# Kernel optimization log

Measured on AMD Instinct MI355X. Metric: run time of the kernel, lower is better.

The kernel has to match this reference:

```python
import jax, jax.numpy as jnp
import numpy as np

B = 32768   # batch (agents)
H = 64      # h_dim
E = 16      # embedding_dim
M = 6       # num_modes (n_samples)
P = M * 2   # traj_points
T = 30      # pred_len (seq_len)


def setup_inputs() -> dict:
    key = jax.random.key(0)
    ks = jax.random.split(key, 14)
    def s(k, shape, scale=0.1):
        return jax.random.normal(k, shape, jnp.float32) * scale
    return dict(
        traj_abs=s(ks[0], (1, B, 2), 1.0),
        traj_rel=s(ks[1], (1, B, 2), 1.0),
        h0=s(ks[2], (1, B, H)),
        c0=s(ks[3], (1, B, H)),
        W_ih=s(ks[4], (4 * H, E)),
        W_hh=s(ks[5], (4 * H, H)),
        b_ih=s(ks[6], (4 * H,)),
        b_hh=s(ks[7], (4 * H,)),
        W_se=s(ks[8], (E, P)),
        b_se=s(ks[9], (E,)),
        W_pos=s(ks[10], (P, H)),
        b_pos=s(ks[11], (P,)),
        W_conf=s(ks[12], (M, H)),
        b_conf=s(ks[13], (M,)),
    )


def reference(traj_abs, traj_rel, h0, c0, W_ih, W_hh, b_ih, b_hh,
              W_se, b_se, W_pos, b_pos, W_conf, b_conf):
    b = traj_rel.shape[1]
    # repeat_interleave the (x,y) pair num_modes times along feature dim -> [b, 12]
    rel12 = jnp.tile(traj_rel.reshape(b, 1, 2), (1, M, 1)).reshape(b, P)
    x = jax.nn.leaky_relu(rel12 @ W_se.T + b_se)  # [b, E]
    h = h0[0]
    c = c0[0]

    def step(carry, _):
        x, h, c = carry
        # PyTorch LSTM cell, gate order i, f, g, o
        gates = x @ W_ih.T + b_ih + h @ W_hh.T + b_hh  # [b, 4H]
        i, f, g, o = jnp.split(gates, 4, axis=-1)
        c = jax.nn.sigmoid(f) * c + jax.nn.sigmoid(i) * jnp.tanh(g)
        h = jax.nn.sigmoid(o) * jnp.tanh(c)
        rel = h @ W_pos.T + b_pos                      # [b, P]
        x = jax.nn.leaky_relu(rel @ W_se.T + b_se)     # [b, E]
        return (x, h, c), rel

    (x, h, c), rels = jax.lax.scan(step, (x, h, c), None, length=T)  # rels: [T, b, P]
    pred = rels.reshape(T, b, M, 2).transpose(1, 2, 0, 3)            # [b, M, T, 2]
    conf = jax.nn.softmax(h @ W_conf.T + b_conf, axis=1)             # [b, M]
    return pred, conf
```

## Files before the change

### kernel.cpp

```cpp
#include <hip/hip_runtime.h>
#include <hip/hip_bf16.h>

typedef _Float16 half8 __attribute__((ext_vector_type(8)));
typedef _Float16 half4 __attribute__((ext_vector_type(4)));
typedef float float4v __attribute__((ext_vector_type(4)));

#define BATCH 32768
#define TT 30

#if __has_builtin(__builtin_amdgcn_exp2f)
#define FEXP2(x) __builtin_amdgcn_exp2f(x)
#else
#define FEXP2(x) __expf((x) * 0.6931471805599453f)
#endif
#if __has_builtin(__builtin_amdgcn_rcpf)
#define FRCP(x) __builtin_amdgcn_rcpf(x)
#else
#define FRCP(x) (1.0f / (x))
#endif

#define NLOG2E  -1.4426950408889634f
#define N2LOG2E -2.8853900817779268f

#define WFRAG_OFF 0
#define WCF_OFF   12288
#define BIASB_OFF 13312
#define SXY_OFF   13568
#define CBIAS_OFF 13616
#define WCONF_OFF 13648
#define BCONF_OFF 14032
#define FLAG_IDX  14038
#define CONF_BASE (BATCH * 360)

__global__ void detect_kernel(const unsigned short* __restrict__ raw,
                              int* __restrict__ flag_out) {
    __shared__ int sflag[256];
    int local = 0;
    for (int i = threadIdx.x; i < 16384; i += 256) {
        unsigned short u = raw[i];
        if ((u & 0x7F80u) == 0x7F80u) local = 1;
    }
    sflag[threadIdx.x] = local;
    __syncthreads();
    if (threadIdx.x == 0) {
        int f = 0;
        for (int i = 0; i < 256; ++i) f |= sflag[i];
        flag_out[0] = f;
    }
}

__device__ __forceinline__ float ldin(const void* p, int i, int isf32) {
    return isf32 ? ((const float*)p)[i]
                 : (float)((const __hip_bfloat16*)p)[i];
}

__global__ void prep_kernel(const void* __restrict__ W_ih,
                            const void* __restrict__ W_hh,
                            const void* __restrict__ b_ih,
                            const void* __restrict__ b_hh,
                            const void* __restrict__ W_se,
                            const void* __restrict__ b_se,
                            const void* __restrict__ W_pos,
                            const void* __restrict__ b_pos,
                            const void* __restrict__ W_conf,
                            const void* __restrict__ b_conf,
                            float* __restrict__ ws)
{
    const int isf32 = ((const int*)(ws + FLAG_IDX))[0];
    int tid = blockIdx.x * blockDim.x + threadIdx.x;
    int stride = gridDim.x * blockDim.x;
    _Float16* wfh = (_Float16*)ws;

    for (int idx = tid; idx < 24576; idx += stride) {
        int jj = idx & 7, r = idx >> 3;
        int lane = r & 63; r >>= 6;
        int ks = r % 3; r /= 3;
        int gate = r & 3; int wv = r >> 2;
        int col = lane & 15, akq = lane >> 4;
        int k = ks * 32 + akq * 8 + jj;
        int row = gate * 64 + wv * 16 + col;
        float v = 0.f;
        if (k < 16) v = ldin(W_ih, row * 16 + k, isf32);
        else if (k < 80) v = ldin(W_hh, row * 64 + (k - 16), isf32);
        v *= (gate == 2) ? N2LOG2E : NLOG2E;
        wfh[idx] = (_Float16)v;
    }
    _Float16* wch = (_Float16*)(ws + WCF_OFF);
    for (int idx = tid; idx < 2048; idx += stride) {
        int jj = idx & 7, r = idx >> 3;
        int lane = r & 63; r >>= 6;
        int ks = r & 1, role = r >> 1;
        int col = lane & 15, akq = lane >> 4;
        int k = ks * 32 + akq * 8 + jj;
        float v = 0.f;
        if (role == 0) {
            if (col < 12) v = ldin(W_pos, col * 64 + k, isf32);
        } else {
            float s = 0.f;
            for (int p = 0; p < 12; ++p)
                s += ldin(W_se, col * 12 + p, isf32) * ldin(W_pos, p * 64 + k, isf32);
            v = s;
        }
        wch[idx] = (_Float16)v;
    }
    for (int idx = tid; idx < 256; idx += stride) {
        int gate = idx >> 6;
        float scale = (gate == 2) ? N2LOG2E : NLOG2E;
        ws[BIASB_OFF + idx] = (ldin(b_ih, idx, isf32) + ldin(b_hh, idx, isf32)) * scale;
    }
    for (int idx = tid; idx < 16; idx += stride) {
        float sx = 0.f, sy = 0.f;
        for (int m = 0; m < 6; ++m) {
            sx += ldin(W_se, idx * 12 + 2 * m, isf32);
            sy += ldin(W_se, idx * 12 + 2 * m + 1, isf32);
        }
        ws[SXY_OFF + idx * 3 + 0] = sx;
        ws[SXY_OFF + idx * 3 + 1] = sy;
        ws[SXY_OFF + idx * 3 + 2] = ldin(b_se, idx, isf32);
    }
    for (int idx = tid; idx < 32; idx += stride) {
        int w = idx >> 4, cc = idx & 15;
        float v = 0.f;
        if (w == 0) {
            if (cc < 12) v = ldin(b_pos, cc, isf32);
        } else {
            float s = ldin(b_se, cc, isf32);
            for (int p = 0; p < 12; ++p)
                s += ldin(W_se, cc * 12 + p, isf32) * ldin(b_pos, p, isf32);
            v = s;
        }
        ws[CBIAS_OFF + idx] = v;
    }
    for (int idx = tid; idx < 384; idx += stride)
        ws[WCONF_OFF + idx] = ldin(W_conf, idx, isf32);
    for (int idx = tid; idx < 6; idx += stride)
        ws[BCONF_OFF + idx] = ldin(b_conf, idx, isf32);
}

__global__ __launch_bounds__(256, 4) void lstm_kernel(
    const void* __restrict__ traj_rel,
    const void* __restrict__ h0,
    const void* __restrict__ c0,
    const float* __restrict__ ws,
    float* __restrict__ out)
{
    __shared__ _Float16 zsh[2 * 16 * 168];
    __shared__ _Float16 predh[12 * 30 * 36];

    const int tid = threadIdx.x;
    const int lane = tid & 63;
    const int wid = __builtin_amdgcn_readfirstlane(tid >> 6);
    const int role = wid & 1;
    const int col16 = lane & 15;
    const int akq = lane >> 4;
    const int base = blockIdx.x * 32;
    const int isf32 = ((const int*)(ws + FLAG_IDX))[0];

    const float4v* wfg = (const float4v*)ws;
    half8 Bf[4][3];
#pragma unroll
    for (int tl = 0; tl < 4; ++tl)
#pragma unroll
        for (int ks = 0; ks < 3; ++ks)
            Bf[tl][ks] = __builtin_bit_cast(half8,
                wfg[((wid * 4 + tl) * 3 + ks) * 64 + lane]);
    float bias4[4];
#pragma unroll
    for (int tl = 0; tl < 4; ++tl)
        bias4[tl] = ws[BIASB_OFF + tl * 64 + wid * 16 + col16];
    half8 wfc[2];
    {
        const float4v* wcg = (const float4v*)(ws + WCF_OFF);
#pragma unroll
        for (int ks = 0; ks < 2; ++ks)
            wfc[ks] = __builtin_bit_cast(half8, wcg[(role * 2 + ks) * 64 + lane]);
    }
    const float cb = ws[CBIAS_OFF + role * 16 + col16];

    int aoff[2][3];
#pragma unroll
    for (int p = 0; p < 2; ++p)
#pragma unroll
        for (int ks = 0; ks < 3; ++ks) {
            int q = ks * 4 + akq;
            int off = (q < 2) ? q * 8
                    : (q < 10) ? 32 + p * 64 + (q - 2) * 8
                               : 16 + (q - 10) * 8;
            aoff[p][ks] = col16 * 168 + off;
        }
    const int zcb = col16 * 168 + 32 + akq * 8;
    const int rb = akq * 672;
    const int hb = 32 + wid * 16 + col16;

    float cg0[4], cg1[4];
    {
        int unit = wid * 16 + col16;
#pragma unroll
        for (int i = 0; i < 4; ++i) {
            cg0[i] = ldin(c0, (base + akq * 4 + i) * 64 + unit, isf32);
            cg1[i] = ldin(c0, (base + 16 + akq * 4 + i) * 64 + unit, isf32);
        }
    }
    {
        int m = tid & 31, jq2 = tid >> 5;
        int g = m >> 4, row = m & 15;
        _Float16* zg = &zsh[g * 2688 + row * 168];
        half8 ha;
#pragma unroll
        for (int i = 0; i < 8; ++i)
            ha[i] = (_Float16)ldin(h0, (base + m) * 64 + jq2 * 8 + i, isf32);
        *(half8*)&zg[32 + jq2 * 8] = ha;
        if (jq2 < 4) {
            float rx = ldin(traj_rel, 2 * (base + m), isf32);
            float ry = ldin(traj_rel, 2 * (base + m) + 1, isf32);
            half4 xs;
#pragma unroll
            for (int i = 0; i < 4; ++i) {
                int e = 4 * jq2 + i;
                float x = fmaf(rx, ws[SXY_OFF + e * 3],
                          fmaf(ry, ws[SXY_OFF + e * 3 + 1], ws[SXY_OFF + e * 3 + 2]));
                xs[i] = (_Float16)(x > 0.f ? x : 0.01f * x);
            }
            *(half4*)&zg[4 * jq2] = xs;
        } else if (jq2 < 6) {
            half8 zz = {};
            *(half8*)&zg[16 + (jq2 - 4) * 8] = zz;
        }
    }
    __syncthreads();

    _Float16* const zg0p = &zsh[0];
    _Float16* const zg1p = &zsh[2688];

#define PHASE_AB(ZG, PC, PN, CARR) do {                                       \
    float4v acc_[4];                                                          \
    _Pragma("unroll")                                                         \
    for (int tl = 0; tl < 4; ++tl) {                                          \
        float bv = bias4[tl];                                                 \
        acc_[tl][0] = bv; acc_[tl][1] = bv; acc_[tl][2] = bv; acc_[tl][3] = bv;\
    }                                                                         \
    _Pragma("unroll")                                                         \
    for (int ks = 0; ks < 3; ++ks) {                                          \
        half8 af_ = *(const half8*)&(ZG)[aoff[PC][ks]];                       \
        _Pragma("unroll")                                                     \
        for (int tl = 0; tl < 4; ++tl)                                        \
            acc_[tl] = __builtin_amdgcn_mfma_f32_16x16x32_f16(                \
                af_, Bf[tl][ks], acc_[tl], 0, 0, 0);                          \
    }                                                                         \
    _Pragma("unroll")                                                         \
    for (int i = 0; i < 4; ++i) {                                             \
        float ei = FEXP2(acc_[0][i]);                                         \
        float ef = FEXP2(acc_[1][i]);                                         \
        float eg = FEXP2(acc_[2][i]);                                         \
        float eo = FEXP2(acc_[3][i]);                                         \
        float pp = (1.f + ei) * (1.f + eg);                                   \
        float qq = 1.f + ef;                                                  \
        float cn = fmaf((CARR)[i], pp, (1.f - eg) * qq) * FRCP(pp * qq);      \
        (CARR)[i] = cn;                                                       \
        float ec = FEXP2(cn * N2LOG2E);                                       \
        float hn = (1.f - ec) * FRCP((1.f + eo) * (1.f + ec));                \
        (ZG)[rb + i * 168 + (PN) * 64 + hb] = (_Float16)hn;                   \
    }                                                                         \
} while (0)

#define PHASE_C(ZG, P, T, GI) do {                                            \
    float4v racc_;                                                            \
    racc_[0] = cb; racc_[1] = cb; racc_[2] = cb; racc_[3] = cb;               \
    _Pragma("unroll")                                                         \
    for (int ks = 0; ks < 2; ++ks) {                                          \
        half8 af_ = *(const half8*)&(ZG)[zcb + (P) * 64 + ks * 32];           \
        racc_ = __builtin_amdgcn_mfma_f32_16x16x32_f16(                       \
            af_, wfc[ks], racc_, 0, 0, 0);                                    \
    }                                                                         \
    if (role == 0) {                                                          \
        if (col16 < 12) {                                                     \
            half4 hv_;                                                        \
            _Pragma("unroll")                                                 \
            for (int i = 0; i < 4; ++i) hv_[i] = (_Float16)racc_[i];          \
            *(half4*)&predh[(col16 * 30 + (T)) * 36 + (GI) * 16 + akq * 4] = hv_;\
        }                                                                     \
    } else if ((T) != TT - 1) {                                               \
        _Pragma("unroll")                                                     \
        for (int i = 0; i < 4; ++i) {                                         \
            float xv_ = racc_[i];                                             \
            xv_ = xv_ > 0.f ? xv_ : 0.01f * xv_;                              \
            (ZG)[rb + i * 168 + col16] = (_Float16)xv_;                       \
        }                                                                     \
    }                                                                         \
} while (0)

    PHASE_AB(zg0p, 0, 1, cg0);
    __syncthreads();
    PHASE_AB(zg1p, 0, 1, cg1);
    if (wid < 2) PHASE_C(zg0p, 1, 0, 0);
    __syncthreads();

    for (int t = 1; t < TT - 1; t += 2) {
        PHASE_AB(zg0p, 1, 0, cg0);
        if (wid >= 2) PHASE_C(zg1p, 1, t - 1, 1);
        __syncthreads();
        PHASE_AB(zg1p, 1, 0, cg1);
        if (wid < 2) PHASE_C(zg0p, 0, t, 0);
        __syncthreads();
        PHASE_AB(zg0p, 0, 1, cg0);
        if (wid >= 2) PHASE_C(zg1p, 0, t, 1);
        __syncthreads();
        PHASE_AB(zg1p, 0, 1, cg1);
        if (wid < 2) PHASE_C(zg0p, 1, t + 1, 0);
        __syncthreads();
    }
    PHASE_AB(zg0p, 1, 0, cg0);
    if (wid >= 2) PHASE_C(zg1p, 1, TT - 2, 1);
    __syncthreads();
    PHASE_AB(zg1p, 1, 0, cg1);
    if (wid < 2) PHASE_C(zg0p, 0, TT - 1, 0);
    __syncthreads();
    if (wid >= 2) PHASE_C(zg1p, 0, TT - 1, 1);
    __syncthreads();

    {
        float4* po4 = (float4*)(out + (size_t)base * 360);
#pragma unroll 1
        for (int q2 = 0; q2 < 12; ++q2) {
            int idx4 = q2 * 256 + tid;
            if (idx4 < 2880) {
                int a = idx4 / 90, rem = idx4 % 90;
                int m = rem / 15, tq = rem % 15;
                int t0 = tq * 2;
                float4 o;
                o.x = (float)predh[((2 * m + 0) * 30 + t0) * 36 + a];
                o.y = (float)predh[((2 * m + 1) * 30 + t0) * 36 + a];
                o.z = (float)predh[((2 * m + 0) * 30 + t0 + 1) * 36 + a];
                o.w = (float)predh[((2 * m + 1) * 30 + t0 + 1) * 36 + a];
                po4[idx4] = o;
            }
        }
    }

    if (wid == 0 && lane < 32) {
        int m = lane;
        int g = m >> 4, row = m & 15;
        float l[6];
#pragma unroll
        for (int md = 0; md < 6; ++md) l[md] = ws[BCONF_OFF + md];
        for (int jj = 0; jj < 64; ++jj) {
            float hv = (float)zsh[g * 2688 + row * 168 + 32 + jj];
#pragma unroll
            for (int md = 0; md < 6; ++md)
                l[md] = fmaf(hv, ws[WCONF_OFF + md * 64 + jj], l[md]);
        }
        float mx = l[0];
#pragma unroll
        for (int md = 1; md < 6; ++md) mx = fmaxf(mx, l[md]);
        float ex[6], s = 0.f;
#pragma unroll
        for (int md = 0; md < 6; ++md) { ex[md] = __expf(l[md] - mx); s += ex[md]; }
        float inv = FRCP(s);
#pragma unroll
        for (int md = 0; md < 6; ++md)
            out[CONF_BASE + (size_t)(base + m) * 6 + md] = ex[md] * inv;
    }
}

extern "C" void kernel_launch(void* const* d_in, const int* in_sizes, int n_in,
                              void* d_out, int out_size, void* d_ws, size_t ws_size,
                              hipStream_t stream) {
    const void* traj_rel = d_in[1];
    const void* h0   = d_in[2];
    const void* c0   = d_in[3];
    const void* W_ih = d_in[4];
    const void* W_hh = d_in[5];
    const void* b_ih = d_in[6];
    const void* b_hh = d_in[7];
    const void* W_se = d_in[8];
    const void* b_se = d_in[9];
    const void* W_pos  = d_in[10];
    const void* b_pos  = d_in[11];
    const void* W_conf = d_in[12];
    const void* b_conf = d_in[13];
    float* ws = (float*)d_ws;
    float* out = (float*)d_out;

    detect_kernel<<<1, 256, 0, stream>>>((const unsigned short*)W_hh,
                                         (int*)(ws + FLAG_IDX));
    prep_kernel<<<40, 256, 0, stream>>>(W_ih, W_hh, b_ih, b_hh, W_se, b_se,
                                        W_pos, b_pos, W_conf, b_conf, ws);
    lstm_kernel<<<BATCH / 32, 256, 0, stream>>>(traj_rel, h0, c0, ws, out);
}
```

Baseline: 196.8 us.

## Transpose MFMA operands, fold LSTM bias into weights, vectorize LDS writes

Swaps the A/B operands of the MFMAs so each lane holds four consecutive hidden units of one batch row. The h, x and prediction results can then be written to LDS as packed half4 stores instead of scattered scalar stores, and the prediction buffer layout changes to match. The gate bias is folded into the weight fragment as an extra K column, paired with a constant 1.0 in the input tile, so the per-gate bias registers go away. The risk is more LDS bank conflicts on the half4 stores, plus the bias now being rounded to fp16.

```diff
diff --git a/kernel.cpp b/kernel.cpp
--- a/kernel.cpp
+++ b/kernel.cpp
@@ -82,6 +82,7 @@
         float v = 0.f;
         if (k < 16) v = ldin(W_ih, row * 16 + k, isf32);
         else if (k < 80) v = ldin(W_hh, row * 64 + (k - 16), isf32);
+        else if (k == 80) v = ldin(b_ih, row, isf32) + ldin(b_hh, row, isf32);
         v *= (gate == 2) ? N2LOG2E : NLOG2E;
         wfh[idx] = (_Float16)v;
     }
@@ -145,7 +146,7 @@
     float* __restrict__ out)
 {
     __shared__ _Float16 zsh[2 * 16 * 168];
-    __shared__ _Float16 predh[12 * 30 * 36];
+    __shared__ _Float16 predh[32 * 30 * 12];
 
     const int tid = threadIdx.x;
     const int lane = tid & 63;
@@ -164,10 +165,6 @@
         for (int ks = 0; ks < 3; ++ks)
             Bf[tl][ks] = __builtin_bit_cast(half8,
                 wfg[((wid * 4 + tl) * 3 + ks) * 64 + lane]);
-    float bias4[4];
-#pragma unroll
-    for (int tl = 0; tl < 4; ++tl)
-        bias4[tl] = ws[BIASB_OFF + tl * 64 + wid * 16 + col16];
     half8 wfc[2];
     {
         const float4v* wcg = (const float4v*)(ws + WCF_OFF);
@@ -175,7 +172,46 @@
         for (int ks = 0; ks < 2; ++ks)
             wfc[ks] = __builtin_bit_cast(half8, wcg[(role * 2 + ks) * 64 + lane]);
     }
-    const float cb = ws[CBIAS_OFF + role * 16 + col16];
+    const float4v cb4 = *(const float4v*)&ws[CBIAS_OFF + role * 16 + akq * 4];
+
+    float cg0[4], cg1[4];
+#pragma unroll
+    for (int i = 0; i < 4; ++i) {
+        int unit = wid * 16 + akq * 4 + i;
+        cg0[i] = ldin(c0, (base + col16) * 64 + unit, isf32);
+        cg1[i] = ldin(c0, (base + 16 + col16) * 64 + unit, isf32);
+    }
+    {
+        int m = tid & 31, jq2 = tid >> 5;
+        int g = m >> 4, row = m & 15;
+        _Float16* zr = &zsh[g * 2688 + row * 168];
+        half8 ha;
+#pragma unroll
+        for (int i = 0; i < 8; ++i)
+            ha[i] = (_Float16)ldin(h0, (base + m) * 64 + jq2 * 8 + i, isf32);
+        *(half8*)&zr[32 + jq2 * 8] = ha;
+        if (jq2 < 4) {
+            float rx = ldin(traj_rel, 2 * (base + m), isf32);
+            float ry = ldin(traj_rel, 2 * (base + m) + 1, isf32);
+            half4 xs;
+#pragma unroll
+            for (int i = 0; i < 4; ++i) {
+                int e = 4 * jq2 + i;
+                float x = fmaf(rx, ws[SXY_OFF + e * 3],
+                          fmaf(ry, ws[SXY_OFF + e * 3 + 1], ws[SXY_OFF + e * 3 + 2]));
+                xs[i] = (_Float16)(x > 0.f ? x : 0.01f * x);
+            }
+            *(half4*)&zr[4 * jq2] = xs;
+        } else if (jq2 == 4) {
+            half8 zz = {};
+            zz[0] = (_Float16)1.0f;
+            *(half8*)&zr[16] = zz;
+        } else if (jq2 == 5) {
+            half8 zz = {};
+            *(half8*)&zr[24] = zz;
+        }
+    }
+    __syncthreads();
 
     int aoff[2][3];
 #pragma unroll
@@ -189,64 +225,26 @@
             aoff[p][ks] = col16 * 168 + off;
         }
     const int zcb = col16 * 168 + 32 + akq * 8;
-    const int rb = akq * 672;
-    const int hb = 32 + wid * 16 + col16;
-
-    float cg0[4], cg1[4];
-    {
-        int unit = wid * 16 + col16;
-#pragma unroll
-        for (int i = 0; i < 4; ++i) {
-            cg0[i] = ldin(c0, (base + akq * 4 + i) * 64 + unit, isf32);
-            cg1[i] = ldin(c0, (base + 16 + akq * 4 + i) * 64 + unit, isf32);
-        }
-    }
-    {
-        int m = tid & 31, jq2 = tid >> 5;
-        int g = m >> 4, row = m & 15;
-        _Float16* zg = &zsh[g * 2688 + row * 168];
-        half8 ha;
-#pragma unroll
-        for (int i = 0; i < 8; ++i)
-            ha[i] = (_Float16)ldin(h0, (base + m) * 64 + jq2 * 8 + i, isf32);
-        *(half8*)&zg[32 + jq2 * 8] = ha;
-        if (jq2 < 4) {
-            float rx = ldin(traj_rel, 2 * (base + m), isf32);
-            float ry = ldin(traj_rel, 2 * (base + m) + 1, isf32);
-            half4 xs;
-#pragma unroll
-            for (int i = 0; i < 4; ++i) {
-                int e = 4 * jq2 + i;
-                float x = fmaf(rx, ws[SXY_OFF + e * 3],
-                          fmaf(ry, ws[SXY_OFF + e * 3 + 1], ws[SXY_OFF + e * 3 + 2]));
-                xs[i] = (_Float16)(x > 0.f ? x : 0.01f * x);
-            }
-            *(half4*)&zg[4 * jq2] = xs;
-        } else if (jq2 < 6) {
-            half8 zz = {};
-            *(half8*)&zg[16 + (jq2 - 4) * 8] = zz;
-        }
-    }
-    __syncthreads();
-
-    _Float16* const zg0p = &zsh[0];
-    _Float16* const zg1p = &zsh[2688];
-
-#define PHASE_AB(ZG, PC, PN, CARR) do {                                       \
+    const int hw4 = col16 * 168 + 32 + wid * 16 + akq * 4;
+    const int xw4 = col16 * 168 + akq * 4;
+
+#define ZG(g) (&zsh[(g) * 2688])
+
+#define PHASE_AB(ZG_, PC, PN, CARR) do {                                      \
     float4v acc_[4];                                                          \
     _Pragma("unroll")                                                         \
-    for (int tl = 0; tl < 4; ++tl) {                                          \
-        float bv = bias4[tl];                                                 \
-        acc_[tl][0] = bv; acc_[tl][1] = bv; acc_[tl][2] = bv; acc_[tl][3] = bv;\
+    for (int g = 0; g < 4; ++g) {                                             \
+        acc_[g][0] = 0.f; acc_[g][1] = 0.f; acc_[g][2] = 0.f; acc_[g][3] = 0.f;\
     }                                                                         \
     _Pragma("unroll")                                                         \
     for (int ks = 0; ks < 3; ++ks) {                                          \
-        half8 af_ = *(const half8*)&(ZG)[aoff[PC][ks]];                       \
+        half8 af_ = *(const half8*)&(ZG_)[aoff[PC][ks]];                      \
         _Pragma("unroll")                                                     \
-        for (int tl = 0; tl < 4; ++tl)                                        \
-            acc_[tl] = __builtin_amdgcn_mfma_f32_16x16x32_f16(                \
-                af_, Bf[tl][ks], acc_[tl], 0, 0, 0);                          \
-    }                                                                         \
+        for (int g = 0; g < 4; ++g)                                           \
+            acc_[g] = __builtin_amdgcn_mfma_f32_16x16x32_f16(                 \
+                Bf[g][ks], af_, acc_[g], 0, 0, 0);                            \
+    }                                                                         \
+    half4 hv_;                                                                \
     _Pragma("unroll")                                                         \
     for (int i = 0; i < 4; ++i) {                                             \
         float ei = FEXP2(acc_[0][i]);                                         \
@@ -259,35 +257,40 @@
         (CARR)[i] = cn;                                                       \
         float ec = FEXP2(cn * N2LOG2E);                                       \
         float hn = (1.f - ec) * FRCP((1.f + eo) * (1.f + ec));                \
-        (ZG)[rb + i * 168 + (PN) * 64 + hb] = (_Float16)hn;                   \
-    }                                                                         \
+        hv_[i] = (_Float16)hn;                                                \
+    }                                                                         \
+    *(half4*)&(ZG_)[hw4 + (PN) * 64] = hv_;                                   \
 } while (0)
 
-#define PHASE_C(ZG, P, T, GI) do {                                            \
+#define PHASE_C(ZG_, P, T, GI) do {                                           \
     float4v racc_;                                                            \
-    racc_[0] = cb; racc_[1] = cb; racc_[2] = cb; racc_[3] = cb;               \
+    racc_[0] = cb4[0]; racc_[1] = cb4[1]; racc_[2] = cb4[2]; racc_[3] = cb4[3];\
     _Pragma("unroll")                                                         \
     for (int ks = 0; ks < 2; ++ks) {                                          \
-        half8 af_ = *(const half8*)&(ZG)[zcb + (P) * 64 + ks * 32];           \
+        half8 af_ = *(const half8*)&(ZG_)[zcb + (P) * 64 + ks * 32];          \
         racc_ = __builtin_amdgcn_mfma_f32_16x16x32_f16(                       \
-            af_, wfc[ks], racc_, 0, 0, 0);                                    \
+            wfc[ks], af_, racc_, 0, 0, 0);                                    \
     }                                                                         \
     if (role == 0) {                                                          \
-        if (col16 < 12) {                                                     \
-            half4 hv_;                                                        \
+        if (akq < 3) {                                                        \
+            half4 pv_;                                                        \
             _Pragma("unroll")                                                 \
-            for (int i = 0; i < 4; ++i) hv_[i] = (_Float16)racc_[i];          \
-            *(half4*)&predh[(col16 * 30 + (T)) * 36 + (GI) * 16 + akq * 4] = hv_;\
+            for (int i = 0; i < 4; ++i) pv_[i] = (_Float16)racc_[i];          \
+            *(half4*)&predh[(((GI) * 16 + col16) * 30 + (T)) * 12 + akq * 4] = pv_;\
         }                                                                     \
     } else if ((T) != TT - 1) {                                               \
+        half4 xv4_;                                                           \
         _Pragma("unroll")                                                     \
         for (int i = 0; i < 4; ++i) {                                         \
             float xv_ = racc_[i];                                             \
-            xv_ = xv_ > 0.f ? xv_ : 0.01f * xv_;                              \
-            (ZG)[rb + i * 168 + col16] = (_Float16)xv_;                       \
+            xv4_[i] = (_Float16)(xv_ > 0.f ? xv_ : 0.01f * xv_);              \
         }                                                                     \
+        *(half4*)&(ZG_)[xw4] = xv4_;                                          \
     }                                                                         \
 } while (0)
+
+    _Float16* const zg0p = ZG(0);
+    _Float16* const zg1p = ZG(1);
 
     PHASE_AB(zg0p, 0, 1, cg0);
     __syncthreads();
@@ -328,10 +331,10 @@
                 int m = rem / 15, tq = rem % 15;
                 int t0 = tq * 2;
                 float4 o;
-                o.x = (float)predh[((2 * m + 0) * 30 + t0) * 36 + a];
-                o.y = (float)predh[((2 * m + 1) * 30 + t0) * 36 + a];
-                o.z = (float)predh[((2 * m + 0) * 30 + t0 + 1) * 36 + a];
-                o.w = (float)predh[((2 * m + 1) * 30 + t0 + 1) * 36 + a];
+                o.x = (float)predh[(a * 30 + t0) * 12 + 2 * m];
+                o.y = (float)predh[(a * 30 + t0) * 12 + 2 * m + 1];
+                o.z = (float)predh[(a * 30 + t0 + 1) * 12 + 2 * m];
+                o.w = (float)predh[(a * 30 + t0 + 1) * 12 + 2 * m + 1];
                 po4[idx4] = o;
             }
         }
```

Result: no change. 197.9 us (+0.6%).
